# Performance work log

Measured on AMD Instinct MI355X. Metric: run time of the kernel, lower is better.

The kernel has to match this reference:

```python
import jax, jax.numpy as jnp
import numpy as np

N = 100000          # num_nodes
E = 600000          # num_edges
NUM_EDGE_TYPE = 10
R = 2 * NUM_EDGE_TYPE  # 20 relations (forward + inverse)
DIN, DH, DOUT = 128, 128, 128


def setup_inputs() -> dict:
    key = jax.random.key(0)
    k = jax.random.split(key, 8)
    glorot = lambda kk, shape: jax.random.normal(kk, shape, jnp.float32) * np.sqrt(2.0 / (shape[-2] + shape[-1]))
    return {
        "x": jnp.arange(N, dtype=jnp.int64) if jax.config.jax_enable_x64 else jnp.arange(N, dtype=jnp.int32),
        "edge": jax.random.randint(k[0], (2, E), 0, N),
        "edge_type": jax.random.randint(k[1], (E,), 0, R),
        "emb": jax.random.normal(k[2], (N, DIN), jnp.float32) * 0.02,
        "w1": glorot(k[3], (R, DIN, DH)),
        "root1": glorot(k[4], (DIN, DH)),
        "b1": jnp.zeros((DH,), jnp.float32),
        "w2": glorot(k[5], (R, DH, DOUT)),
        "root2": glorot(k[6], (DH, DOUT)),
        "b2": jnp.zeros((DOUT,), jnp.float32),
    }


def rgcn_conv(h, edge, edge_type, w, root, b):
    # PyG RGCNConv: out = sum_r mean_{j in N_r(i)} W_r x_j + root x_i + b
    src, dst = edge[0], edge[1]
    x_src = h[src]                       # [E, din] gathered source features
    out = h @ root + b                   # root/self transform
    for r in range(R):                   # fixed structural loop over relations
        m = (edge_type == r).astype(h.dtype)                       # [E]
        s = jax.ops.segment_sum(x_src * m[:, None], dst, num_segments=N)  # [N, din]
        c = jax.ops.segment_sum(m, dst, num_segments=N)            # [N] in-degree per relation
        mean = s / jnp.clip(c, 1.0)[:, None]
        out = out + mean @ w[r]          # linear => mean-then-transform == transform-then-mean
    return out


def reference(x, edge, edge_type, emb, w1, root1, b1, w2, root2, b2):
    h = emb[x]                                        # embedding lookup [N, DIN]
    h1 = rgcn_conv(h, edge, edge_type, w1, root1, b1)  # [N, DH]
    h = jax.nn.relu(h1)
    h2 = rgcn_conv(h, edge, edge_type, w2, root2, b2)  # [N, DOUT]
    return h2
```

## Files before the change

kernel.cpp:

```cpp
#include <hip/hip_runtime.h>

#define DD 128
#define RNUM 20

typedef __attribute__((ext_vector_type(4))) float f32x4;
typedef __attribute__((ext_vector_type(8))) short s16x8;
typedef unsigned long long u64;
typedef unsigned int u32;

__device__ inline ushort f2bf(float f) {
    unsigned u = __float_as_uint(f);
    unsigned r = (u + 0x7FFF + ((u >> 16) & 1)) >> 16;
    return (ushort)r;
}

#define M_RCNT 0
#define M_RBASE 20
#define M_RTILE 41
#define M_TOT 88
#define BRSTRIDE 2048


__global__ void k_transpose(const float* w1, const float* root1,
                            const float* w2, const float* root2,
                            ushort* wt1, ushort* wt2) {
    int m = blockIdx.x;
    const float* src;
    ushort* dst;
    if (m < 21) { src = (m == 20) ? root1 : w1 + m * DD * DD; dst = wt1 + m * DD * DD; }
    else { int mm = m - 21; src = (mm == 20) ? root2 : w2 + mm * DD * DD; dst = wt2 + mm * DD * DD; }
    for (int idx = threadIdx.x; idx < DD * DD; idx += blockDim.x) {
        int n = idx >> 7, k = idx & 127;
        dst[idx] = f2bf(src[k * DD + n]);
    }
}

__global__ void k_gather_h(const int* x, const float* emb, ushort* h, int N) {
    int id = blockIdx.x * blockDim.x + threadIdx.x;
    if (id >= N * 32) return;
    int n = id >> 5, c = (id & 31) * 4;
    int xn = x[n];
    float4 v = *(const float4*)(emb + (size_t)xn * DD + c);
    ushort4 o;
    o.x = f2bf(v.x); o.y = f2bf(v.y); o.z = f2bf(v.z); o.w = f2bf(v.w);
    *(ushort4*)(h + (size_t)n * DD + c) = o;
}


__global__ void k_hist(const int* edge, const int* et, int E, u32* cnt) {
    int e = blockIdx.x * 256 + threadIdx.x;
    if (e >= E) return;
    int b = edge[E + e] * RNUM + et[e];
    atomicAdd(&cnt[b], 1u);
}

__global__ __launch_bounds__(256) void k_scan_part(const u32* cnt, int NB, u64* psum, u32* blockrel) {
    __shared__ u64 red[256];
    __shared__ u32 h20[RNUM];
    int t = threadIdx.x;
    if (t < RNUM) h20[t] = 0;
    __syncthreads();
    int base = blockIdx.x * 1024 + t * 4;
    u64 s = 0;
    for (int i = 0; i < 4; i++) {
        int b = base + i;
        if (b < NB) {
            u32 c = cnt[b];
            s += (u64)c | ((u64)(c > 0) << 32);
            if (c) atomicAdd(&h20[b % RNUM], 1u);
        }
    }
    red[t] = s;
    __syncthreads();
    for (int o = 128; o > 0; o >>= 1) {
        if (t < o) red[t] += red[t + o];
        __syncthreads();
    }
    if (t == 0) psum[blockIdx.x] = red[0];
    if (t < RNUM) blockrel[t * BRSTRIDE + blockIdx.x] = h20[t];
}

__global__ __launch_bounds__(256) void k_scan_top(u64* psum, int P, u32* meta,
                                                  u64* escan, int NB, u32* segoff, int N) {
    __shared__ u64 sc[256];
    int t = threadIdx.x;
    u64 loc[8];
    u64 s = 0;
    for (int i = 0; i < 8; i++) {
        int p = t * 8 + i;
        loc[i] = (p < P) ? psum[p] : 0;
        s += loc[i];
    }
    sc[t] = s;
    __syncthreads();
    for (int o = 1; o < 256; o <<= 1) {
        u64 x = (t >= o) ? sc[t - o] : 0;
        __syncthreads();
        sc[t] += x;
        __syncthreads();
    }
    u64 run = sc[t] - s;
    for (int i = 0; i < 8; i++) {
        int p = t * 8 + i;
        if (p < P) { psum[p] = run; run += loc[i]; }
    }
    if (t == 255) {
        u64 tot = sc[255];
        *(u64*)(meta + M_TOT) = tot;
        escan[NB] = tot;
        segoff[N] = (u32)(tot >> 32);
    }
}

__global__ __launch_bounds__(256) void k_scan_add(const u32* cnt, int NB, const u64* psum,
                                                  u64* escan, u32* segoff) {
    __shared__ u64 sc[256];
    int t = threadIdx.x;
    int base = blockIdx.x * 1024 + t * 4;
    u64 v[4];
    u64 s = 0;
    for (int i = 0; i < 4; i++) {
        int b = base + i;
        u32 c = (b < NB) ? cnt[b] : 0;
        v[i] = (u64)c | ((u64)(c > 0) << 32);
        s += v[i];
    }
    sc[t] = s;
    __syncthreads();
    for (int o = 1; o < 256; o <<= 1) {
        u64 x = (t >= o) ? sc[t - o] : 0;
        __syncthreads();
        sc[t] += x;
        __syncthreads();
    }
    u64 run = psum[blockIdx.x] + sc[t] - s;
    for (int i = 0; i < 4; i++) {
        int b = base + i;
        if (b < NB) {
            escan[b] = run;
            if (b % RNUM == 0) segoff[b / RNUM] = (u32)(run >> 32);
            run += v[i];
        }
    }
}

__global__ __launch_bounds__(256) void k_colscan2(u32* blockrel, int P, u32* meta) {
    __shared__ u32 sc[256];
    int c = blockIdx.x;
    int t = threadIdx.x;
    u32* col = blockrel + c * BRSTRIDE;
    u32 v[8];
    u32 s = 0;
#pragma unroll
    for (int i = 0; i < 8; i++) {
        int p = t * 8 + i;
        v[i] = (p < P) ? col[p] : 0;
        s += v[i];
    }
    sc[t] = s;
    __syncthreads();
    for (int o = 1; o < 256; o <<= 1) {
        u32 x = (t >= o) ? sc[t - o] : 0;
        __syncthreads();
        sc[t] += x;
        __syncthreads();
    }
    u32 run = sc[t] - s;
#pragma unroll
    for (int i = 0; i < 8; i++) {
        int p = t * 8 + i;
        if (p < P) { col[p] = run; run += v[i]; }
    }
    if (t == 255) meta[M_RCNT + c] = sc[255];
}

__global__ void k_rscan(u32* meta) {
    if (threadIdx.x || blockIdx.x) return;
    u32 off = 0, toff = 0;
    for (int r = 0; r < RNUM; r++) {
        meta[M_RBASE + r] = off;
        meta[M_RTILE + r] = toff;
        u32 c = meta[M_RCNT + r];
        off += c;
        toff += (c + 63) >> 6;
    }
    meta[M_RBASE + RNUM] = off;
    meta[M_RTILE + RNUM] = toff;
}

__global__ __launch_bounds__(256) void k_build(const u32* cnt, const u64* escan, int NB,
                                               const u32* __restrict__ meta,
                                               const u32* __restrict__ blockrel,
                                               u32* segmeta, u32* rseg) {
    __shared__ u32 h20[RNUM];
    int t = threadIdx.x;
    if (t < RNUM) h20[t] = 0;
    __syncthreads();
    int base = blockIdx.x * 1024 + t * 4;
    for (int i = 0; i < 4; i++) {
        int b = base + i;
        if (b >= NB) break;
        u32 c = cnt[b];
        if (!c) continue;
        int r = b % RNUM;
        u32 my = atomicAdd(&h20[r], 1u);
        u64 e = escan[b];
        u32 s = (u32)(e >> 32);
        segmeta[s] = ((u32)e & 0xFFFFFu) | (c << 20);
        rseg[meta[M_RBASE + r] + blockrel[r * BRSTRIDE + blockIdx.x] + my] = s;
    }
}

__global__ void k_scatter2(const int* edge, const int* et, int E,
                           const u64* escan, u32* cnt, int* bsrc2) {
    int e = blockIdx.x * 256 + threadIdx.x;
    if (e >= E) return;
    int b = edge[E + e] * RNUM + et[e];
    u32 old = atomicSub(&cnt[b], 1u);
    u32 pos = (u32)escan[b] + old - 1;
    bsrc2[pos] = edge[e];
}


__global__ __launch_bounds__(256) void k_agg_gemm(const ushort* __restrict__ h,
                                                  const ushort* __restrict__ wt,
                                                  const int* __restrict__ bsrc2,
                                                  const u32* __restrict__ segmeta,
                                                  const u32* __restrict__ rseg,
                                                  const u32* __restrict__ meta,
                                                  ushort* __restrict__ Y) {
    __shared__ __align__(16) ushort Al[64 * 136];
    __shared__ __align__(16) ushort Bl[128 * 136];
    __shared__ int ssid[64];
    int tile = blockIdx.x;
    if (tile >= (int)meta[M_RTILE + RNUM]) return;
    int r = 0;
#pragma unroll
    for (int i = 1; i < RNUM; i++)
        if (tile >= (int)meta[M_RTILE + i]) r = i;
    int j0 = (tile - (int)meta[M_RTILE + r]) * 64;
    int nseg = (int)meta[M_RCNT + r];
    u32 rb = meta[M_RBASE + r];
    int t = threadIdx.x;
    int j = t >> 2, t4 = t & 3;
    {
        float a[32];
#pragma unroll
        for (int i = 0; i < 32; i++) a[i] = 0.f;
        int sj = j0 + j;
        int s = -1;
        if (sj < nseg) {
            s = (int)rseg[rb + sj];
            u32 m = segmeta[s];
            int epos = m & 0xFFFFF;
            int c = (int)(m >> 20);
            for (int q = 0; q < c; q++) {
                int src = bsrc2[epos + q];
                const ushort* hp = h + (size_t)src * DD + t4 * 32;
#pragma unroll
                for (int k = 0; k < 4; k++) {
                    s16x8 v = *(const s16x8*)(hp + k * 8);
#pragma unroll
                    for (int i = 0; i < 8; i++)
                        a[k * 8 + i] += __uint_as_float(((u32)(ushort)v[i]) << 16);
                }
            }
            float inv = 1.0f / (float)c;
#pragma unroll
            for (int i = 0; i < 32; i++) a[i] *= inv;
        }
        if (t4 == 0) ssid[j] = s;
        ushort* arow = Al + j * 136 + t4 * 32;
#pragma unroll
        for (int k = 0; k < 4; k++) {
            s16x8 o;
#pragma unroll
            for (int i = 0; i < 8; i++) o[i] = (short)f2bf(a[k * 8 + i]);
            *(s16x8*)(arow + k * 8) = o;
        }
    }
    const ushort* wr = wt + (size_t)r * DD * DD;
    for (int q = t; q < 2048; q += 256) {
        int n = q >> 4, cb = q & 15;
        int4 v = *(const int4*)(wr + (size_t)n * DD + cb * 8);
        *(int4*)((char*)Bl + n * 272 + cb * 16) = v;
    }
    __syncthreads();
    int w = t >> 6, l = t & 63, lr = l & 15, lg = l >> 4;
    f32x4 acc[8];
#pragma unroll
    for (int c = 0; c < 8; c++) acc[c] = (f32x4){0.f, 0.f, 0.f, 0.f};
#pragma unroll
    for (int ks = 0; ks < 4; ks++) {
        s16x8 af = *(const s16x8*)((const char*)Al + (w * 16 + lr) * 272 + ks * 64 + lg * 16);
#pragma unroll
        for (int c = 0; c < 8; c++) {
            s16x8 bf = *(const s16x8*)((const char*)Bl + (c * 16 + lr) * 272 + ks * 64 + lg * 16);
            acc[c] = __builtin_amdgcn_mfma_f32_16x16x32_bf16(af, bf, acc[c], 0, 0, 0);
        }
    }
#pragma unroll
    for (int q = 0; q < 4; q++) {
        int row = w * 16 + lg * 4 + q;
        int s = ssid[row];
        if (s < 0) continue;
        ushort* yp = Y + (size_t)s * DD;
#pragma unroll
        for (int c8 = 0; c8 < 8; c8++) {
            int col = c8 * 16 + lr;
            yp[col] = f2bf(acc[c8][q]);
        }
    }
}

template <int RELU>
__global__ __launch_bounds__(256) void k_out(const ushort* __restrict__ h,
                                             const ushort* __restrict__ wroot,
                                             const float* __restrict__ bias,
                                             const ushort* __restrict__ Y,
                                             const u32* __restrict__ segoff,
                                             ushort* __restrict__ hout,
                                             float* __restrict__ fout, int N) {
    __shared__ __align__(16) char U[64 * 272 + 128 * 272];
    ushort* Al = (ushort*)U;
    ushort* Bl = (ushort*)(U + 64 * 272);
    float* Cl = (float*)U;
    __shared__ float biasl[DD];
    int n0 = blockIdx.x * 64;
    int t = threadIdx.x;
    if (t < DD) biasl[t] = bias[t];
    for (int q = t; q < 1024; q += 256) {
        int row = q >> 4, cb = q & 15;
        int i = n0 + row;
        int4 v = make_int4(0, 0, 0, 0);
        if (i < N) v = *(const int4*)(h + (size_t)i * DD + cb * 8);
        *(int4*)((char*)Al + row * 272 + cb * 16) = v;
    }
    for (int q = t; q < 2048; q += 256) {
        int n = q >> 4, cb = q & 15;
        int4 v = *(const int4*)(wroot + (size_t)n * DD + cb * 8);
        *(int4*)((char*)Bl + n * 272 + cb * 16) = v;
    }
    __syncthreads();
    int w = t >> 6, l = t & 63, lr = l & 15, lg = l >> 4;
    f32x4 acc[8];
#pragma unroll
    for (int c = 0; c < 8; c++) acc[c] = (f32x4){0.f, 0.f, 0.f, 0.f};
#pragma unroll
    for (int ks = 0; ks < 4; ks++) {
        s16x8 af = *(const s16x8*)((const char*)Al + (w * 16 + lr) * 272 + ks * 64 + lg * 16);
#pragma unroll
        for (int c = 0; c < 8; c++) {
            s16x8 bf = *(const s16x8*)((const char*)Bl + (c * 16 + lr) * 272 + ks * 64 + lg * 16);
            acc[c] = __builtin_amdgcn_mfma_f32_16x16x32_bf16(af, bf, acc[c], 0, 0, 0);
        }
    }
    __syncthreads();
#pragma unroll
    for (int q = 0; q < 4; q++) {
        int row = w * 16 + lg * 4 + q;
#pragma unroll
        for (int c8 = 0; c8 < 8; c8++) Cl[row * 132 + c8 * 16 + lr] = acc[c8][q];
    }
    __syncthreads();
    int j = t >> 2, t4 = t & 3;
    int node = n0 + j;
    if (node >= N) return;
    float a[32];
#pragma unroll
    for (int k = 0; k < 8; k++) {
        f32x4 cv = *(const f32x4*)(Cl + j * 132 + t4 * 32 + k * 4);
        a[k * 4 + 0] = cv[0]; a[k * 4 + 1] = cv[1]; a[k * 4 + 2] = cv[2]; a[k * 4 + 3] = cv[3];
    }
    u32 s0 = segoff[node], s1 = segoff[node + 1];
    for (u32 s = s0; s < s1; s++) {
        const ushort* yp = Y + (size_t)s * DD + t4 * 32;
#pragma unroll
        for (int k = 0; k < 4; k++) {
            s16x8 v = *(const s16x8*)(yp + k * 8);
#pragma unroll
            for (int i = 0; i < 8; i++)
                a[k * 8 + i] += __uint_as_float(((u32)(ushort)v[i]) << 16);
        }
    }
#pragma unroll
    for (int i = 0; i < 32; i++) a[i] += biasl[t4 * 32 + i];
    if (RELU) {
        ushort* op = hout + (size_t)node * DD + t4 * 32;
#pragma unroll
        for (int k = 0; k < 4; k++) {
            s16x8 o;
#pragma unroll
            for (int i = 0; i < 8; i++) {
                float xv = a[k * 8 + i];
                o[i] = (short)f2bf(xv > 0.f ? xv : 0.f);
            }
            *(s16x8*)(op + k * 8) = o;
        }
    } else {
#pragma unroll
        for (int k = 0; k < 8; k++) {
            f32x4 o = (f32x4){a[k * 4 + 0], a[k * 4 + 1], a[k * 4 + 2], a[k * 4 + 3]};
            *(f32x4*)(fout + (size_t)node * DD + t4 * 32 + k * 4) = o;
        }
    }
}


extern "C" void kernel_launch(void* const* d_in, const int* in_sizes, int n_in,
                              void* d_out, int out_size, void* d_ws, size_t ws_size,
                              hipStream_t stream) {
    const int* x = (const int*)d_in[0];
    const int* edge = (const int*)d_in[1];
    const int* etype = (const int*)d_in[2];
    const float* emb = (const float*)d_in[3];
    const float* w1 = (const float*)d_in[4];
    const float* root1 = (const float*)d_in[5];
    const float* b1 = (const float*)d_in[6];
    const float* w2 = (const float*)d_in[7];
    const float* root2 = (const float*)d_in[8];
    const float* b2 = (const float*)d_in[9];
    float* out = (float*)d_out;

    const int N = in_sizes[0];
    const int E = in_sizes[2];
    const int NB = N * RNUM;

    char* p = (char*)d_ws;
    auto alloc = [&](size_t bytes) {
        char* q = p;
        p += (bytes + 255) & ~(size_t)255;
        return q;
    };
    int* bsrc2 = (int*)alloc((size_t)E * 4);
    u32* segmeta = (u32*)alloc((size_t)E * 4);
    u32* rseg = (u32*)alloc((size_t)E * 4);
    u32* segoff = (u32*)alloc((size_t)(N + 1) * 4);
    u32* meta = (u32*)alloc(512);
    u32* blockrel = (u32*)alloc((size_t)RNUM * BRSTRIDE * 4);
    ushort* wt1 = (ushort*)alloc((size_t)21 * DD * DD * 2);
    ushort* wt2 = (ushort*)alloc((size_t)21 * DD * DD * 2);
    ushort* hbuf = (ushort*)alloc((size_t)N * DD * 2);
    u64* escan = (u64*)alloc((size_t)(NB + 1) * 8);
    u32* cnt = (u32*)alloc((size_t)NB * 4);
    u64* psum = (u64*)alloc(2048 * 8);
    ushort* Y = (ushort*)escan;
    {
        char* yend = (char*)escan + (size_t)E * DD * 2;
        if (yend > p) p = yend;
    }

    hipMemsetAsync(cnt, 0, (size_t)NB * 4, stream);
    hipMemsetAsync(meta, 0, 512, stream);

    int blkE = (E + 255) / 256;
    int blkH = (N * 32 + 255) / 256;
    int P = (NB + 1023) / 1024;
    int TILES = (E + 63) / 64 + RNUM;
    int blkOut = (N + 63) / 64;

    k_transpose<<<42, 256, 0, stream>>>(w1, root1, w2, root2, wt1, wt2);
    k_gather_h<<<blkH, 256, 0, stream>>>(x, emb, hbuf, N);
    k_hist<<<blkE, 256, 0, stream>>>(edge, etype, E, cnt);
    k_scan_part<<<P, 256, 0, stream>>>(cnt, NB, psum, blockrel);
    k_scan_top<<<1, 256, 0, stream>>>(psum, P, meta, escan, NB, segoff, N);
    k_scan_add<<<P, 256, 0, stream>>>(cnt, NB, psum, escan, segoff);
    k_colscan2<<<RNUM, 256, 0, stream>>>(blockrel, P, meta);
    k_rscan<<<1, 64, 0, stream>>>(meta);
    k_build<<<P, 256, 0, stream>>>(cnt, escan, NB, meta, blockrel, segmeta, rseg);
    k_scatter2<<<blkE, 256, 0, stream>>>(edge, etype, E, escan, cnt, bsrc2);

    k_agg_gemm<<<TILES, 256, 0, stream>>>(hbuf, wt1, bsrc2, segmeta, rseg, meta, Y);
    k_out<1><<<blkOut, 256, 0, stream>>>(hbuf, wt1 + 20 * DD * DD, b1, Y, segoff, hbuf, nullptr, N);

    k_agg_gemm<<<TILES, 256, 0, stream>>>(hbuf, wt2, bsrc2, segmeta, rseg, meta, Y);
    k_out<0><<<blkOut, 256, 0, stream>>>(hbuf, wt2 + 20 * DD * DD, b2, Y, segoff, nullptr, out, N);
}
```

Before: 489.7 us.

## Drop LDS weight staging, swizzle A tile, fast-path single-edge segments

Both MFMA kernels stop staging the 128x128 bf16 weight matrix in LDS and read B fragments straight from global memory (L2/L1 cached). The A tile moves to an unpadded 256-byte-row layout with an XOR swizzle to avoid bank conflicts. The aggregation kernel gets a fast path for single-edge segments that copies bf16 directly without fp32 accumulate and reconvert. Launch bounds hint 6 and 4 waves per block. This cuts LDS footprint to raise occupancy and removes the weight-load barrier, at the cost of repeated global weight reads per wave.

```diff
diff --git a/kernel.cpp b/kernel.cpp
--- a/kernel.cpp
+++ b/kernel.cpp
@@ -222,15 +222,14 @@
 }
 
 
-__global__ __launch_bounds__(256) void k_agg_gemm(const ushort* __restrict__ h,
-                                                  const ushort* __restrict__ wt,
-                                                  const int* __restrict__ bsrc2,
-                                                  const u32* __restrict__ segmeta,
-                                                  const u32* __restrict__ rseg,
-                                                  const u32* __restrict__ meta,
-                                                  ushort* __restrict__ Y) {
-    __shared__ __align__(16) ushort Al[64 * 136];
-    __shared__ __align__(16) ushort Bl[128 * 136];
+__global__ __launch_bounds__(256, 6) void k_agg_gemm(const ushort* __restrict__ h,
+                                                     const ushort* __restrict__ wt,
+                                                     const int* __restrict__ bsrc2,
+                                                     const u32* __restrict__ segmeta,
+                                                     const u32* __restrict__ rseg,
+                                                     const u32* __restrict__ meta,
+                                                     ushort* __restrict__ Y) {
+    __shared__ __align__(16) char Al[64 * 256];
     __shared__ int ssid[64];
     int tile = blockIdx.x;
     if (tile >= (int)meta[M_RTILE + RNUM]) return;
@@ -244,16 +243,30 @@
     int t = threadIdx.x;
     int j = t >> 2, t4 = t & 3;
     {
-        float a[32];
-#pragma unroll
-        for (int i = 0; i < 32; i++) a[i] = 0.f;
+        char* arow = Al + j * 256;
+        int swz = (j & 7) << 4;
         int sj = j0 + j;
         int s = -1;
+        int c = 0, epos = 0;
         if (sj < nseg) {
             s = (int)rseg[rb + sj];
             u32 m = segmeta[s];
-            int epos = m & 0xFFFFF;
-            int c = (int)(m >> 20);
+            epos = m & 0xFFFFF;
+            c = (int)(m >> 20);
+        }
+        if (t4 == 0) ssid[j] = s;
+        if (c == 1) {
+            int src = bsrc2[epos];
+            const ushort* hp = h + (size_t)src * DD + t4 * 32;
+#pragma unroll
+            for (int k = 0; k < 4; k++) {
+                s16x8 v = *(const s16x8*)(hp + k * 8);
+                *(s16x8*)(arow + ((t4 * 64 + k * 16) ^ swz)) = v;
+            }
+        } else {
+            float a[32];
+#pragma unroll
+            for (int i = 0; i < 32; i++) a[i] = 0.f;
             for (int q = 0; q < c; q++) {
                 int src = bsrc2[epos + q];
                 const ushort* hp = h + (size_t)src * DD + t4 * 32;
@@ -265,38 +278,31 @@
                         a[k * 8 + i] += __uint_as_float(((u32)(ushort)v[i]) << 16);
                 }
             }
-            float inv = 1.0f / (float)c;
+            float inv = (c > 0) ? (1.0f / (float)c) : 0.f;
 #pragma unroll
             for (int i = 0; i < 32; i++) a[i] *= inv;
-        }
-        if (t4 == 0) ssid[j] = s;
-        ushort* arow = Al + j * 136 + t4 * 32;
-#pragma unroll
-        for (int k = 0; k < 4; k++) {
-            s16x8 o;
-#pragma unroll
-            for (int i = 0; i < 8; i++) o[i] = (short)f2bf(a[k * 8 + i]);
-            *(s16x8*)(arow + k * 8) = o;
-        }
-    }
+#pragma unroll
+            for (int k = 0; k < 4; k++) {
+                s16x8 o;
+#pragma unroll
+                for (int i = 0; i < 8; i++) o[i] = (short)f2bf(a[k * 8 + i]);
+                *(s16x8*)(arow + ((t4 * 64 + k * 16) ^ swz)) = o;
+            }
+        }
+    }
+    __syncthreads();
+    int w = t >> 6, l = t & 63, lr = l & 15, lg = l >> 4;
     const ushort* wr = wt + (size_t)r * DD * DD;
-    for (int q = t; q < 2048; q += 256) {
-        int n = q >> 4, cb = q & 15;
-        int4 v = *(const int4*)(wr + (size_t)n * DD + cb * 8);
-        *(int4*)((char*)Bl + n * 272 + cb * 16) = v;
-    }
-    __syncthreads();
-    int w = t >> 6, l = t & 63, lr = l & 15, lg = l >> 4;
     f32x4 acc[8];
 #pragma unroll
-    for (int c = 0; c < 8; c++) acc[c] = (f32x4){0.f, 0.f, 0.f, 0.f};
+    for (int c8 = 0; c8 < 8; c8++) acc[c8] = (f32x4){0.f, 0.f, 0.f, 0.f};
 #pragma unroll
     for (int ks = 0; ks < 4; ks++) {
-        s16x8 af = *(const s16x8*)((const char*)Al + (w * 16 + lr) * 272 + ks * 64 + lg * 16);
-#pragma unroll
-        for (int c = 0; c < 8; c++) {
-            s16x8 bf = *(const s16x8*)((const char*)Bl + (c * 16 + lr) * 272 + ks * 64 + lg * 16);
-            acc[c] = __builtin_amdgcn_mfma_f32_16x16x32_bf16(af, bf, acc[c], 0, 0, 0);
+        s16x8 af = *(const s16x8*)(Al + (w * 16 + lr) * 256 + ((ks * 64 + lg * 16) ^ ((lr & 7) << 4)));
+#pragma unroll
+        for (int c8 = 0; c8 < 8; c8++) {
+            s16x8 bf = *(const s16x8*)(wr + (size_t)(c8 * 16 + lr) * DD + ks * 32 + lg * 8);
+            acc[c8] = __builtin_amdgcn_mfma_f32_16x16x32_bf16(af, bf, acc[c8], 0, 0, 0);
         }
     }
 #pragma unroll
@@ -314,16 +320,14 @@
 }
 
 template <int RELU>
-__global__ __launch_bounds__(256) void k_out(const ushort* __restrict__ h,
-                                             const ushort* __restrict__ wroot,
-                                             const float* __restrict__ bias,
-                                             const ushort* __restrict__ Y,
-                                             const u32* __restrict__ segoff,
-                                             ushort* __restrict__ hout,
-                                             float* __restrict__ fout, int N) {
-    __shared__ __align__(16) char U[64 * 272 + 128 * 272];
-    ushort* Al = (ushort*)U;
-    ushort* Bl = (ushort*)(U + 64 * 272);
+__global__ __launch_bounds__(256, 4) void k_out(const ushort* __restrict__ h,
+                                                const ushort* __restrict__ wroot,
+                                                const float* __restrict__ bias,
+                                                const ushort* __restrict__ Y,
+                                                const u32* __restrict__ segoff,
+                                                ushort* __restrict__ hout,
+                                                float* __restrict__ fout, int N) {
+    __shared__ __align__(16) char U[64 * 132 * 4];
     float* Cl = (float*)U;
     __shared__ float biasl[DD];
     int n0 = blockIdx.x * 64;
@@ -334,25 +338,20 @@
         int i = n0 + row;
         int4 v = make_int4(0, 0, 0, 0);
         if (i < N) v = *(const int4*)(h + (size_t)i * DD + cb * 8);
-        *(int4*)((char*)Al + row * 272 + cb * 16) = v;
-    }
-    for (int q = t; q < 2048; q += 256) {
-        int n = q >> 4, cb = q & 15;
-        int4 v = *(const int4*)(wroot + (size_t)n * DD + cb * 8);
-        *(int4*)((char*)Bl + n * 272 + cb * 16) = v;
+        *(int4*)(U + row * 256 + ((cb * 16) ^ ((row & 7) << 4))) = v;
     }
     __syncthreads();
     int w = t >> 6, l = t & 63, lr = l & 15, lg = l >> 4;
     f32x4 acc[8];
 #pragma unroll
-    for (int c = 0; c < 8; c++) acc[c] = (f32x4){0.f, 0.f, 0.f, 0.f};
+    for (int c8 = 0; c8 < 8; c8++) acc[c8] = (f32x4){0.f, 0.f, 0.f, 0.f};
 #pragma unroll
     for (int ks = 0; ks < 4; ks++) {
-        s16x8 af = *(const s16x8*)((const char*)Al + (w * 16 + lr) * 272 + ks * 64 + lg * 16);
-#pragma unroll
-        for (int c = 0; c < 8; c++) {
-            s16x8 bf = *(const s16x8*)((const char*)Bl + (c * 16 + lr) * 272 + ks * 64 + lg * 16);
-            acc[c] = __builtin_amdgcn_mfma_f32_16x16x32_bf16(af, bf, acc[c], 0, 0, 0);
+        s16x8 af = *(const s16x8*)(U + (w * 16 + lr) * 256 + ((ks * 64 + lg * 16) ^ ((lr & 7) << 4)));
+#pragma unroll
+        for (int c8 = 0; c8 < 8; c8++) {
+            s16x8 bf = *(const s16x8*)(wroot + (size_t)(c8 * 16 + lr) * DD + ks * 32 + lg * 8);
+            acc[c8] = __builtin_amdgcn_mfma_f32_16x16x32_bf16(af, bf, acc[c8], 0, 0, 0);
         }
     }
     __syncthreads();
```

Result: slower. 651.3 us (+33.0%).
